# Kernel optimization log

Hardware: AMD Instinct MI355X
Metric: run time of the kernel (lower is better)

The kernel has to match this reference:

```python
import jax, jax.numpy as jnp
import numpy as np

N, C, HW, HEADS = 2048, 16, 8, 4
F = C * HW * HW  # 1024
E = 16384
EPS = 1e-5
NEG_SLOPE = 0.2


def _bn(x, g, b):
    # training-mode BatchNorm2d over (N, H, W)
    m = x.mean(axis=(0, 2, 3), keepdims=True)
    v = x.var(axis=(0, 2, 3), keepdims=True)
    return (x - m) * jax.lax.rsqrt(v + EPS) * g[None, :, None, None] + b[None, :, None, None]


def _conv1x1(x, w, b):
    # 1x1 conv == per-pixel linear: w is [out_c, in_c]
    return jnp.einsum('nchw,oc->nohw', x, w) + b[None, :, None, None]


def _gatv2(xf, edge_index, wl, bl, wr, br, att, bias_gat):
    # xf: [N, F] node features
    xl = (xf @ wl + bl).reshape(N, HEADS, F)  # source-side transform (lin_l)
    xr = (xf @ wr + br).reshape(N, HEADS, F)  # target-side transform (lin_r)
    src, dst = edge_index[0], edge_index[1]
    loops = jnp.arange(N)
    # PyG default: remove existing self loops (mask them) then add self loops
    src_f = jnp.concatenate([src, loops])
    dst_f = jnp.concatenate([dst, loops])
    valid = jnp.concatenate([src != dst, jnp.ones((N,), bool)])
    xj = xl[src_f]                                   # [E+N, HEADS, F] gather
    e = jax.nn.leaky_relu(xj + xr[dst_f], negative_slope=NEG_SLOPE)
    logits = jnp.einsum('ehf,hf->eh', e, att)        # [E+N, HEADS]
    logits = jnp.where(valid[:, None], logits, -jnp.inf)
    mx = jax.lax.stop_gradient(jax.ops.segment_max(logits, dst_f, num_segments=N))
    expv = jnp.where(valid[:, None], jnp.exp(logits - mx[dst_f]), 0.0)
    denom = jax.ops.segment_sum(expv, dst_f, num_segments=N)
    alpha = expv / denom[dst_f]                      # segment softmax over incoming edges
    out = jax.ops.segment_sum(alpha[:, :, None] * xj, dst_f, num_segments=N)  # [N, HEADS, F]
    return out.reshape(N, HEADS * F) + bias_gat


def setup_inputs() -> dict:
    key = jax.random.key(0)
    ks = jax.random.split(key, 8)
    s = 0.02
    return {
        'x': jax.random.normal(ks[0], (N, C, HW, HW), jnp.float32),
        'edge_index': jax.random.randint(ks[1], (2, E), 0, N),
        'w1': jax.random.normal(ks[2], (C, C), jnp.float32) * s,
        'b1': jnp.zeros((C,), jnp.float32),
        'g1': jnp.ones((C,), jnp.float32),
        'be1': jnp.zeros((C,), jnp.float32),
        'wl': jax.random.normal(ks[3], (F, HEADS * F), jnp.float32) * s,
        'bl': jnp.zeros((HEADS * F,), jnp.float32),
        'wr': jax.random.normal(ks[4], (F, HEADS * F), jnp.float32) * s,
        'br': jnp.zeros((HEADS * F,), jnp.float32),
        'att': jax.random.normal(ks[5], (HEADS, F), jnp.float32) * s,
        'bias_gat': jnp.zeros((HEADS * F,), jnp.float32),
        'w2': jax.random.normal(ks[6], (C, HEADS * C), jnp.float32) * s,
        'b2': jnp.zeros((C,), jnp.float32),
        'g2': jnp.ones((C,), jnp.float32),
        'be2': jnp.zeros((C,), jnp.float32),
    }


def reference(x, edge_index, w1, b1, g1, be1, wl, bl, wr, br, att, bias_gat, w2, b2, g2, be2):
    res = x
    y = _bn(_conv1x1(x, w1, b1), g1, be1)            # fc1: Conv2d 1x1 + BN
    yf = y.reshape(N, F)
    g = _gatv2(yf, edge_index, wl, bl, wr, br, att, bias_gat)
    g = g.reshape(N, HEADS * C, HW, HW)
    out = _bn(_conv1x1(g, w2, b2), g2, be2)          # fc2: Conv2d 1x1 + BN
    return out + res                                  # DropPath(0.0) == Identity
```

## Files before the change

### kernel.cpp

```cpp
#include <hip/hip_runtime.h>
#include <stdint.h>

#define N_NODES 2048
#define F_DIM   1024
#define HEADS   4
#define NF      4096
#define ROW     8192
#define E_EDGES 16384
#define MAXE    (E_EDGES + N_NODES)
#define BN_EPS  1e-5f
#define NSLOPE  0.2f

typedef unsigned short ushort_t;
typedef __attribute__((ext_vector_type(8))) short bf16x8;
typedef __attribute__((ext_vector_type(4))) float f32x4;
typedef __attribute__((ext_vector_type(8))) unsigned short us8;

__device__ __forceinline__ float b2f(unsigned short u) {
    union { unsigned int i; float f; } x; x.i = ((unsigned int)u) << 16; return x.f;
}
__device__ __forceinline__ unsigned short f2b(float f) {
    union { float f; unsigned int i; } x; x.f = f;
    unsigned int r = x.i + 0x7fffu + ((x.i >> 16) & 1u);
    return (unsigned short)(r >> 16);
}
__device__ __forceinline__ ushort_t ld_canon(const void* src, size_t i, int f32) {
    return f32 ? f2b(((const float*)src)[i]) : ((const ushort_t*)src)[i];
}
__device__ __forceinline__ float ld_f(const void* src, size_t i, int f32) {
    return f32 ? ((const float*)src)[i] : b2f(((const ushort_t*)src)[i]);
}

__device__ __forceinline__ int sniff_f32_blk(const ushort_t* xu, int* lds_flag) {
    int t = threadIdx.x;
    if (t < 64) {
        unsigned e = (xu[2 * t] >> 7) & 0xFF;
        unsigned long long m = __ballot(e >= 0x90u);
        if (t == 0) *lds_flag = (__popcll(m) >= 3) ? 1 : 0;
    }
    __syncthreads();
    return *lds_flag;
}
__device__ __forceinline__ int sniff_i64_blk(const int* ei_raw, int* lds_flag) {
    int t = threadIdx.x;
    if (t < 64) {
        unsigned long long m = __ballot(ei_raw[2 * t + 1] != 0);
        if (t == 0) *lds_flag = (m == 0ull) ? 1 : 0;
    }
    __syncthreads();
    return *lds_flag;
}

__global__ __launch_bounds__(256) void k_prep(
    const void* __restrict__ wl, const void* __restrict__ wr,
    const int* __restrict__ ei_raw, const ushort_t* __restrict__ xu,
    const void* __restrict__ x, const void* __restrict__ w1, const void* __restrict__ b1,
    const void* __restrict__ att, const void* __restrict__ bg,
    ushort_t* __restrict__ wT, int* __restrict__ counts,
    ushort_t* __restrict__ y0b, float* __restrict__ ps, float* __restrict__ pq,
    float* __restrict__ attf, float* __restrict__ bgf)
{
    __shared__ ushort_t tl[64][72];
    __shared__ float xs[1024];
    __shared__ float sw[256];
    __shared__ float sb[16];
    __shared__ int sfl;
    int b = blockIdx.x, t = threadIdx.x;
    if (b >= 2376) {
        int f32 = sniff_f32_blk(xu, &sfl);
        const void* src = (b == 2376) ? att : bg;
        float* dst = (b == 2376) ? attf : bgf;
        #pragma unroll
        for (int j = 0; j < 16; ++j) {
            int idx = t * 16 + j;
            dst[idx] = ld_f(src, idx, f32);
        }
    } else if (b < 2048) {
        int f32 = sniff_f32_blk(xu, &sfl);
        int z = b >> 10, rem = b & 1023;
        int bx = (rem & 63) * 64, by = (rem >> 6) * 64;
        const void* in = z ? wr : wl;
        ushort_t* outT = wT + (size_t)z * 4194304ull;
        #pragma unroll
        for (int i = 0; i < 2; ++i) {
            int idx = t + i * 256;
            int r = idx >> 3, c8 = (idx & 7) * 8;
            size_t gi = (size_t)(by + r) * 4096 + bx + c8;
            us8 v;
            if (f32) {
                const float* fp = (const float*)in + gi;
                float4 a = *(const float4*)fp;
                float4 bb = *(const float4*)(fp + 4);
                v[0] = f2b(a.x); v[1] = f2b(a.y); v[2] = f2b(a.z); v[3] = f2b(a.w);
                v[4] = f2b(bb.x); v[5] = f2b(bb.y); v[6] = f2b(bb.z); v[7] = f2b(bb.w);
            } else {
                v = *(const us8*)((const ushort_t*)in + gi);
            }
            *(us8*)(&tl[r][c8]) = v;
        }
        __syncthreads();
        #pragma unroll
        for (int i = 0; i < 2; ++i) {
            int idx = t + i * 256;
            int rr = idx >> 3, cc8 = (idx & 7) * 8;
            us8 v;
            #pragma unroll
            for (int j = 0; j < 8; ++j) v[j] = tl[cc8 + j][rr];
            *(us8*)(outT + (size_t)(bx + rr) * 1024 + by + cc8) = v;
        }
    } else if (b < 2120) {
        int i64 = sniff_i64_blk(ei_raw, &sfl);
        int idx = (b - 2048) * 256 + t;
        if (idx < E_EDGES) {
            int s = i64 ? ei_raw[2 * idx] : ei_raw[idx];
            int d = i64 ? ei_raw[2 * (E_EDGES + idx)] : ei_raw[E_EDGES + idx];
            if (s != d) atomicAdd(&counts[d], 1);
        } else if (idx < MAXE) {
            atomicAdd(&counts[idx - E_EDGES], 1);
        }
    } else {
        int bid = b - 2120;
        int f32 = sniff_f32_blk(xu, &sfl);
        sw[t] = ld_f(w1, t, f32);
        if (t < 16) sb[t] = ld_f(b1, t, f32);
        int wave = t >> 6, lane = t & 63;
        float s[4] = {0,0,0,0}, q[4] = {0,0,0,0};
        for (int nn = 0; nn < 8; ++nn) {
            int n = bid * 8 + nn;
            __syncthreads();
            #pragma unroll
            for (int i = 0; i < 4; ++i) {
                int idx = t + i * 256;
                xs[idx] = ld_f(x, (size_t)n * 1024 + idx, f32);
            }
            __syncthreads();
            #pragma unroll
            for (int i = 0; i < 4; ++i) {
                int o = wave * 4 + i;
                float acc = sb[o];
                #pragma unroll
                for (int c = 0; c < 16; ++c) acc += xs[c * 64 + lane] * sw[o * 16 + c];
                y0b[(size_t)n * 1024 + o * 64 + lane] = f2b(acc);
                s[i] += acc; q[i] += acc * acc;
            }
        }
        #pragma unroll
        for (int i = 0; i < 4; ++i)
            for (int mm = 1; mm < 64; mm <<= 1) {
                s[i] += __shfl_xor(s[i], mm);
                q[i] += __shfl_xor(q[i], mm);
            }
        if (lane == 0)
            #pragma unroll
            for (int i = 0; i < 4; ++i) {
                ps[bid * 16 + wave * 4 + i] = s[i];
                pq[bid * 16 + wave * 4 + i] = q[i];
            }
    }
}

__global__ __launch_bounds__(256) void k_scatnorm(
    const int* __restrict__ ei_raw, const int* __restrict__ counts,
    int* __restrict__ cursor, int* __restrict__ offs, int* __restrict__ esrc,
    const ushort_t* __restrict__ y0b,
    const float* __restrict__ ps, const float* __restrict__ pq,
    const void* __restrict__ g1, const void* __restrict__ be1,
    const ushort_t* __restrict__ xu, ushort_t* __restrict__ xf)
{
    __shared__ int offl[2048];
    __shared__ int ts[256];
    __shared__ int sfl;
    __shared__ float red[2][64];
    __shared__ float scs[16], shs[16];
    int t = threadIdx.x;
    if (blockIdx.x < 72) {
        int i64 = sniff_i64_blk(ei_raw, &sfl);
        int loc[8]; int tot = 0;
        #pragma unroll
        for (int j = 0; j < 8; ++j) { loc[j] = counts[t * 8 + j]; tot += loc[j]; }
        ts[t] = tot; __syncthreads();
        for (int s = 1; s < 256; s <<= 1) {
            int v = (t >= s) ? ts[t - s] : 0;
            __syncthreads();
            ts[t] += v;
            __syncthreads();
        }
        int run = ts[t] - tot;
        #pragma unroll
        for (int j = 0; j < 8; ++j) { offl[t * 8 + j] = run; run += loc[j]; }
        __syncthreads();
        if (blockIdx.x == 0) {
            #pragma unroll
            for (int j = 0; j < 8; ++j) offs[t * 8 + j] = offl[t * 8 + j];
            if (t == 255) offs[2048] = run;
        }
        int idx = blockIdx.x * 256 + t;
        if (idx < E_EDGES) {
            int s = i64 ? ei_raw[2 * idx] : ei_raw[idx];
            int d = i64 ? ei_raw[2 * (E_EDGES + idx)] : ei_raw[E_EDGES + idx];
            if (s != d) esrc[offl[d] + atomicAdd(&cursor[d], 1)] = s;
        } else if (idx < MAXE) {
            int n = idx - E_EDGES;
            esrc[offl[n] + atomicAdd(&cursor[n], 1)] = n;
        }
    } else {
        int f32 = sniff_f32_blk(xu, &sfl);
        int lane = t & 63, wv = t >> 6;
        float s = 0.f, q = 0.f;
        #pragma unroll
        for (int i = 0; i < 16; ++i) { s += ps[i * 256 + t]; q += pq[i * 256 + t]; }
        s += __shfl_xor(s, 16); q += __shfl_xor(q, 16);
        s += __shfl_xor(s, 32); q += __shfl_xor(q, 32);
        if (lane < 16) { red[0][wv * 16 + lane] = s; red[1][wv * 16 + lane] = q; }
        __syncthreads();
        if (t < 16) {
            float S = red[0][t] + red[0][16 + t] + red[0][32 + t] + red[0][48 + t];
            float Q = red[1][t] + red[1][16 + t] + red[1][32 + t] + red[1][48 + t];
            const float inv = 1.0f / 131072.0f;
            float mean = S * inv;
            float var  = Q * inv - mean * mean;
            float sc = ld_f(g1, t, f32) * rsqrtf(var + BN_EPS);
            scs[t] = sc;
            shs[t] = ld_f(be1, t, f32) - mean * sc;
        }
        __syncthreads();
        size_t base = (size_t)(blockIdx.x - 72) * 4096 + t * 16;
        int ch = ((int)(base >> 6)) & 15;
        float sc = scs[ch], sh = shs[ch];
        us8 v0 = *(const us8*)(y0b + base), v1 = *(const us8*)(y0b + base + 8);
        us8 o0, o1;
        #pragma unroll
        for (int j = 0; j < 8; ++j) {
            o0[j] = f2b(b2f(v0[j]) * sc + sh);
            o1[j] = f2b(b2f(v1[j]) * sc + sh);
        }
        *(us8*)(xf + base) = o0;
        *(us8*)(xf + base + 8) = o1;
    }
}

__global__ __launch_bounds__(256) void k_gemm(
    const ushort_t* __restrict__ A, const ushort_t* __restrict__ BT,
    const void* __restrict__ blr, const void* __restrict__ brr,
    const ushort_t* __restrict__ xu, ushort_t* __restrict__ out)
{
    __shared__ __align__(16) ushort_t smem[16384];
    ushort_t* As0 = smem;
    ushort_t* As1 = smem + 4096;
    ushort_t* Bs0 = smem + 8192;
    ushort_t* Bs1 = smem + 12288;
    ushort_t* cs  = smem;
    __shared__ int sfl;
    int f32 = sniff_f32_blk(xu, &sfl);
    int tid = threadIdx.x;
    int wv = tid >> 6, ln = tid & 63;
    int fid = blockIdx.y * 64 + blockIdx.x;
    int xcd = fid & 7, idx = fid >> 3;
    int m0 = (((xcd & 1) * 8) + (idx & 7)) * 128;
    int n0 = (((xcd >> 1) * 16) + (idx >> 3)) * 128;
    int wm = (wv >> 1) * 64, wn = (wv & 1) * 64;
    int lr = ln & 15, quad = ln >> 4;
    int swz8 = (quad ^ ((lr >> 1) & 3)) * 8;

    f32x4 acc[4][4];
    #pragma unroll
    for (int i = 0; i < 4; ++i)
        #pragma unroll
        for (int j2 = 0; j2 < 4; ++j2) acc[i][j2] = (f32x4){0.f, 0.f, 0.f, 0.f};

    for (int k0 = 0; k0 < 1024; k0 += 64) {
        #pragma unroll
        for (int i = 0; i < 2; ++i) {
            int cbase = i * 256 + wv * 64;
            int ci = cbase + ln;
            int m = ci >> 2, kc = ci & 3;
            int kq = kc ^ ((m >> 1) & 3);
            const ushort_t* ga = A + (size_t)(m0 + m) * 1024 + k0 + kq * 8;
            __builtin_amdgcn_global_load_lds(
                (const __attribute__((address_space(1))) void*)ga,
                (__attribute__((address_space(3))) void*)(&As0[cbase * 8]), 16, 0, 0);
            __builtin_amdgcn_global_load_lds(
                (const __attribute__((address_space(1))) void*)(ga + 32),
                (__attribute__((address_space(3))) void*)(&As1[cbase * 8]), 16, 0, 0);
            const ushort_t* gb = BT + (size_t)(n0 + m) * 1024 + k0 + kq * 8;
            __builtin_amdgcn_global_load_lds(
                (const __attribute__((address_space(1))) void*)gb,
                (__attribute__((address_space(3))) void*)(&Bs0[cbase * 8]), 16, 0, 0);
            __builtin_amdgcn_global_load_lds(
                (const __attribute__((address_space(1))) void*)(gb + 32),
                (__attribute__((address_space(3))) void*)(&Bs1[cbase * 8]), 16, 0, 0);
        }
        __syncthreads();
        #pragma unroll
        for (int p = 0; p < 2; ++p) {
            const ushort_t* Ap = p ? As1 : As0;
            const ushort_t* Bp = p ? Bs1 : Bs0;
            bf16x8 af[4], bfr[4];
            #pragma unroll
            for (int i = 0; i < 4; ++i)
                af[i] = *(const bf16x8*)(&Ap[(wm + i * 16 + lr) * 32 + swz8]);
            #pragma unroll
            for (int j2 = 0; j2 < 4; ++j2)
                bfr[j2] = *(const bf16x8*)(&Bp[(wn + j2 * 16 + lr) * 32 + swz8]);
            #pragma unroll
            for (int i = 0; i < 4; ++i)
                #pragma unroll
                for (int j2 = 0; j2 < 4; ++j2)
                    acc[i][j2] = __builtin_amdgcn_mfma_f32_16x16x32_bf16(af[i], bfr[j2], acc[i][j2], 0, 0, 0);
        }
        __syncthreads();
    }
    float bj[4];
    #pragma unroll
    for (int j2 = 0; j2 < 4; ++j2) {
        int colg = n0 + wn + j2 * 16 + lr;
        bj[j2] = (colg < 4096) ? ld_f(blr, colg, f32) : ld_f(brr, colg - 4096, f32);
    }
    #pragma unroll
    for (int ph = 0; ph < 2; ++ph) {
        if ((wv >> 1) == ph) {
            #pragma unroll
            for (int i = 0; i < 4; ++i)
                #pragma unroll
                for (int j2 = 0; j2 < 4; ++j2) {
                    int col = wn + j2 * 16 + lr;
                    #pragma unroll
                    for (int r = 0; r < 4; ++r)
                        cs[(i * 16 + quad * 4 + r) * 136 + col] = f2b(acc[i][j2][r] + bj[j2]);
                }
        }
        __syncthreads();
        #pragma unroll
        for (int rr = 0; rr < 4; ++rr) {
            int slot = rr * 256 + tid;
            int row = slot >> 4, seg = slot & 15;
            us8 v = *(const us8*)&cs[row * 136 + seg * 8];
            *(us8*)(out + (size_t)(m0 + ph * 64 + row) * ROW + n0 + seg * 8) = v;
        }
        __syncthreads();
    }
}

__global__ __launch_bounds__(64) void k_gat(
    const ushort_t* __restrict__ xlr,
    const float* __restrict__ attf, const float* __restrict__ bgf,
    const int* __restrict__ offsets, const int* __restrict__ esrc,
    ushort_t* __restrict__ g)
{
    int bx = blockIdx.x;
    int h = bx & 3;
    int dbase = (bx >> 2) * 4;
    int l = threadIdx.x;
    size_t hF = (size_t)h * F_DIM + l * 16;

    float attv[16], bgv[16];
    {
        const float* ap = attf + hF;
        const float* bp = bgf + hF;
        float4 a0 = *(const float4*)ap,       a1 = *(const float4*)(ap + 4);
        float4 a2 = *(const float4*)(ap + 8), a3 = *(const float4*)(ap + 12);
        float4 b0 = *(const float4*)bp,       b1 = *(const float4*)(bp + 4);
        float4 b2 = *(const float4*)(bp + 8), b3 = *(const float4*)(bp + 12);
        attv[0]=a0.x; attv[1]=a0.y; attv[2]=a0.z; attv[3]=a0.w;
        attv[4]=a1.x; attv[5]=a1.y; attv[6]=a1.z; attv[7]=a1.w;
        attv[8]=a2.x; attv[9]=a2.y; attv[10]=a2.z; attv[11]=a2.w;
        attv[12]=a3.x; attv[13]=a3.y; attv[14]=a3.z; attv[15]=a3.w;
        bgv[0]=b0.x; bgv[1]=b0.y; bgv[2]=b0.z; bgv[3]=b0.w;
        bgv[4]=b1.x; bgv[5]=b1.y; bgv[6]=b1.z; bgv[7]=b1.w;
        bgv[8]=b2.x; bgv[9]=b2.y; bgv[10]=b2.z; bgv[11]=b2.w;
        bgv[12]=b3.x; bgv[13]=b3.y; bgv[14]=b3.z; bgv[15]=b3.w;
    }

    for (int dd = 0; dd < 4; ++dd) {
        int d = dbase + dd;
        int off = offsets[d], deg = offsets[d + 1] - off;

        float xrv[16];
        {
            const ushort_t* xp = xlr + ((size_t)d * ROW + NF + hF);
            us8 x0 = *(const us8*)xp, x1 = *(const us8*)(xp + 8);
            #pragma unroll
            for (int j = 0; j < 8; ++j) { xrv[j] = b2f(x0[j]); xrv[8 + j] = b2f(x1[j]); }
        }
        float acc[16];
        #pragma unroll
        for (int j = 0; j < 16; ++j) acc[j] = 0.f;
        float s_run = 0.f;

        for (int c0 = 0; c0 < deg; c0 += 64) {
            int cnt = min(64, deg - c0);
            int eidx = esrc[off + c0 + (l < cnt ? l : 0)];
            int e = 0;
            for (; e + 3 < cnt; e += 4) {
                int i0 = __shfl(eidx, e),     i1 = __shfl(eidx, e + 1);
                int i2 = __shfl(eidx, e + 2), i3 = __shfl(eidx, e + 3);
                const ushort_t* p0 = xlr + ((size_t)i0 * ROW + hF);
                const ushort_t* p1 = xlr + ((size_t)i1 * ROW + hF);
                const ushort_t* p2 = xlr + ((size_t)i2 * ROW + hF);
                const ushort_t* p3 = xlr + ((size_t)i3 * ROW + hF);
                us8 v0[4], v1[4];
                v0[0] = *(const us8*)p0; v1[0] = *(const us8*)(p0 + 8);
                v0[1] = *(const us8*)p1; v1[1] = *(const us8*)(p1 + 8);
                v0[2] = *(const us8*)p2; v1[2] = *(const us8*)(p2 + 8);
                v0[3] = *(const us8*)p3; v1[3] = *(const us8*)(p3 + 8);
                float tt[4];
                #pragma unroll
                for (int k = 0; k < 4; ++k) {
                    float t0 = 0.f;
                    #pragma unroll
                    for (int j = 0; j < 8; ++j) {
                        float u;
                        u = b2f(v0[k][j]) + xrv[j];     u = u > 0.f ? u : NSLOPE * u; t0 += u * attv[j];
                        u = b2f(v1[k][j]) + xrv[8 + j]; u = u > 0.f ? u : NSLOPE * u; t0 += u * attv[8 + j];
                    }
                    tt[k] = t0;
                }
                #pragma unroll
                for (int mm = 1; mm < 64; mm <<= 1) {
                    tt[0] += __shfl_xor(tt[0], mm);
                    tt[1] += __shfl_xor(tt[1], mm);
                    tt[2] += __shfl_xor(tt[2], mm);
                    tt[3] += __shfl_xor(tt[3], mm);
                }
                float w0 = __expf(tt[0]), w1 = __expf(tt[1]);
                float w2v = __expf(tt[2]), w3 = __expf(tt[3]);
                s_run += w0 + w1 + w2v + w3;
                #pragma unroll
                for (int j = 0; j < 8; ++j) {
                    acc[j]     += w0 * b2f(v0[0][j]) + w1 * b2f(v0[1][j])
                                + w2v * b2f(v0[2][j]) + w3 * b2f(v0[3][j]);
                    acc[8 + j] += w0 * b2f(v1[0][j]) + w1 * b2f(v1[1][j])
                                + w2v * b2f(v1[2][j]) + w3 * b2f(v1[3][j]);
                }
            }
            for (; e < cnt; ++e) {
                int i0 = __shfl(eidx, e);
                const ushort_t* p = xlr + ((size_t)i0 * ROW + hF);
                us8 a0 = *(const us8*)p, a1 = *(const us8*)(p + 8);
                float t0 = 0.f;
                #pragma unroll
                for (int j = 0; j < 8; ++j) {
                    float u;
                    u = b2f(a0[j]) + xrv[j];     u = u > 0.f ? u : NSLOPE * u; t0 += u * attv[j];
                    u = b2f(a1[j]) + xrv[8 + j]; u = u > 0.f ? u : NSLOPE * u; t0 += u * attv[8 + j];
                }
                #pragma unroll
                for (int mm = 1; mm < 64; mm <<= 1) t0 += __shfl_xor(t0, mm);
                float w0 = __expf(t0);
                s_run += w0;
                #pragma unroll
                for (int j = 0; j < 8; ++j) {
                    acc[j]     += w0 * b2f(a0[j]);
                    acc[8 + j] += w0 * b2f(a1[j]);
                }
            }
        }
        float inv = 1.0f / s_run;
        ushort_t* gp = g + ((size_t)d * NF + hF);
        us8 outv0, outv1;
        #pragma unroll
        for (int j = 0; j < 8; ++j) {
            outv0[j] = f2b(acc[j] * inv + bgv[j]);
            outv1[j] = f2b(acc[8 + j] * inv + bgv[8 + j]);
        }
        *(us8*)gp = outv0;
        *(us8*)(gp + 8) = outv1;
    }
}

__global__ __launch_bounds__(256) void k_fc2(
    const ushort_t* __restrict__ g, const void* __restrict__ w2, const void* __restrict__ b2,
    const ushort_t* __restrict__ xu,
    ushort_t* __restrict__ zb, float* __restrict__ ps, float* __restrict__ pq)
{
    __shared__ float gs[4096];
    __shared__ float sw[1024];
    __shared__ float sb[16];
    __shared__ int sfl;
    int f32 = sniff_f32_blk(xu, &sfl);
    int tid = threadIdx.x;
    #pragma unroll
    for (int i = 0; i < 4; ++i) sw[tid + i * 256] = ld_f(w2, tid + i * 256, f32);
    if (tid < 16) sb[tid] = ld_f(b2, tid, f32);
    int wave = tid >> 6, lane = tid & 63;
    float s[4] = {0,0,0,0}, q[4] = {0,0,0,0};
    for (int nn = 0; nn < 2; ++nn) {
        int n = blockIdx.x * 2 + nn;
        __syncthreads();
        {
            const ushort_t* gp = g + (size_t)n * 4096 + tid * 16;
            us8 v0 = *(const us8*)gp, v1 = *(const us8*)(gp + 8);
            #pragma unroll
            for (int j = 0; j < 8; ++j) {
                gs[tid * 16 + j] = b2f(v0[j]);
                gs[tid * 16 + 8 + j] = b2f(v1[j]);
            }
        }
        __syncthreads();
        float acc[4];
        #pragma unroll
        for (int i = 0; i < 4; ++i) acc[i] = sb[wave * 4 + i];
        #pragma unroll 8
        for (int k = 0; k < 64; ++k) {
            float gv = gs[k * 64 + lane];
            #pragma unroll
            for (int i = 0; i < 4; ++i)
                acc[i] += gv * sw[(wave * 4 + i) * 64 + k];
        }
        #pragma unroll
        for (int i = 0; i < 4; ++i) {
            zb[(size_t)n * 1024 + (wave * 4 + i) * 64 + lane] = f2b(acc[i]);
            s[i] += acc[i]; q[i] += acc[i] * acc[i];
        }
    }
    #pragma unroll
    for (int i = 0; i < 4; ++i)
        for (int mm = 1; mm < 64; mm <<= 1) {
            s[i] += __shfl_xor(s[i], mm);
            q[i] += __shfl_xor(q[i], mm);
        }
    if (lane == 0)
        #pragma unroll
        for (int i = 0; i < 4; ++i) {
            ps[blockIdx.x * 16 + wave * 4 + i] = s[i];
            pq[blockIdx.x * 16 + wave * 4 + i] = q[i];
        }
}

__global__ __launch_bounds__(256) void k_out(
    const ushort_t* __restrict__ zb, const void* __restrict__ x,
    const float* __restrict__ ps, const float* __restrict__ pq,
    const void* __restrict__ g2, const void* __restrict__ be2,
    void* __restrict__ out)
{
    __shared__ float red[2][64];
    __shared__ float scs[16], shs[16];
    __shared__ int sfl;
    int f32 = sniff_f32_blk((const ushort_t*)x, &sfl);
    int t = threadIdx.x, lane = t & 63, wv = t >> 6;
    float s = 0.f, q = 0.f;
    #pragma unroll
    for (int i = 0; i < 64; ++i) { s += ps[i * 256 + t]; q += pq[i * 256 + t]; }
    s += __shfl_xor(s, 16); q += __shfl_xor(q, 16);
    s += __shfl_xor(s, 32); q += __shfl_xor(q, 32);
    if (lane < 16) { red[0][wv * 16 + lane] = s; red[1][wv * 16 + lane] = q; }
    __syncthreads();
    if (t < 16) {
        float S = red[0][t] + red[0][16 + t] + red[0][32 + t] + red[0][48 + t];
        float Q = red[1][t] + red[1][16 + t] + red[1][32 + t] + red[1][48 + t];
        const float inv = 1.0f / 131072.0f;
        float mean = S * inv;
        float var  = Q * inv - mean * mean;
        float sc = ld_f(g2, t, f32) * rsqrtf(var + BN_EPS);
        scs[t] = sc;
        shs[t] = ld_f(be2, t, f32) - mean * sc;
    }
    __syncthreads();
    size_t base = (size_t)blockIdx.x * 4096;
    #pragma unroll
    for (int i = 0; i < 16; ++i) {
        size_t k = base + t + i * 256;
        int ch = ((int)k >> 6) & 15;
        float val = b2f(zb[k]) * scs[ch] + shs[ch] + ld_f(x, k, f32);
        if (f32) ((float*)out)[k] = val;
        else     ((ushort_t*)out)[k] = f2b(val);
    }
}

extern "C" void kernel_launch(void* const* d_in, const int* in_sizes, int n_in,
                              void* d_out, int out_size, void* d_ws, size_t ws_size,
                              hipStream_t stream)
{
    const void* x   = d_in[0];
    const void* ei  = d_in[1];
    const void* w1  = d_in[2];
    const void* b1  = d_in[3];
    const void* g1  = d_in[4];
    const void* be1 = d_in[5];
    const void* wl  = d_in[6];
    const void* bl  = d_in[7];
    const void* wr  = d_in[8];
    const void* br  = d_in[9];
    const void* att = d_in[10];
    const void* bg  = d_in[11];
    const void* w2  = d_in[12];
    const void* b2  = d_in[13];
    const void* g2  = d_in[14];
    const void* be2 = d_in[15];
    (void)in_sizes; (void)n_in; (void)out_size; (void)ws_size;

    char* wsb = (char*)d_ws;
    size_t o = 0;
    auto alloc = [&](size_t bytes) -> void* {
        void* p = wsb + o;
        o = (o + bytes + 255) & ~(size_t)255;
        return p;
    };
    ushort_t* y0b   = (ushort_t*)alloc(2097152ull * 2);
    ushort_t* xf    = (ushort_t*)alloc(2097152ull * 2);
    ushort_t* zb    = (ushort_t*)alloc(2097152ull * 2);
    ushort_t* wT    = (ushort_t*)alloc(8388608ull * 2);
    ushort_t* gbuf  = wT;
    ushort_t* xlr   = (ushort_t*)alloc(16777216ull * 2);
    float* p1s = (float*)alloc(256 * 16 * 4);
    float* p1q = (float*)alloc(256 * 16 * 4);
    float* p2s = (float*)alloc(1024 * 16 * 4);
    float* p2q = (float*)alloc(1024 * 16 * 4);
    int* counts = (int*)alloc(2048 * 4);
    int* cursor = (int*)alloc(2048 * 4);
    int* offs   = (int*)alloc(2049 * 4);
    int* esrc   = (int*)alloc(MAXE * 4);
    float* attf = (float*)alloc(4096 * 4);
    float* bgf  = (float*)alloc(4096 * 4);

    hipMemsetAsync(counts, 0, 2 * 2048 * 4, stream);
    k_prep<<<2378, 256, 0, stream>>>(wl, wr, (const int*)ei, (const ushort_t*)x,
                                     x, w1, b1, att, bg, wT, counts, y0b, p1s, p1q, attf, bgf);
    k_scatnorm<<<584, 256, 0, stream>>>((const int*)ei, counts, cursor, offs, esrc,
                                        y0b, p1s, p1q, g1, be1, (const ushort_t*)x, xf);
    k_gemm<<<dim3(64, 16), 256, 0, stream>>>(xf, wT, bl, br, (const ushort_t*)x, xlr);
    k_gat<<<2048, 64, 0, stream>>>(xlr, attf, bgf, offs, esrc, gbuf);
    k_fc2<<<1024, 256, 0, stream>>>(gbuf, w2, b2, (const ushort_t*)x, zb, p2s, p2q);
    k_out<<<512, 256, 0, stream>>>(zb, x, p2s, p2q, g2, be2, d_out);
}
```

Baseline: 245.4 us.

## Double-buffer GEMM k-loop so next tile loads overlap MFMA compute

```diff
diff --git a/kernel.cpp b/kernel.cpp
--- a/kernel.cpp
+++ b/kernel.cpp
@@ -245,11 +245,7 @@
     const ushort_t* __restrict__ xu, ushort_t* __restrict__ out)
 {
     __shared__ __align__(16) ushort_t smem[16384];
-    ushort_t* As0 = smem;
-    ushort_t* As1 = smem + 4096;
-    ushort_t* Bs0 = smem + 8192;
-    ushort_t* Bs1 = smem + 12288;
-    ushort_t* cs  = smem;
+    ushort_t* cs = smem;
     __shared__ int sfl;
     int f32 = sniff_f32_blk(xu, &sfl);
     int tid = threadIdx.x;
@@ -268,48 +264,52 @@
         #pragma unroll
         for (int j2 = 0; j2 < 4; ++j2) acc[i][j2] = (f32x4){0.f, 0.f, 0.f, 0.f};
 
-    for (int k0 = 0; k0 < 1024; k0 += 64) {
+    auto stage = [&](int tt, int bsel) {
+        ushort_t* Ab = smem + bsel * 8192;
+        ushort_t* Bb = Ab + 4096;
         #pragma unroll
         for (int i = 0; i < 2; ++i) {
             int cbase = i * 256 + wv * 64;
             int ci = cbase + ln;
-            int m = ci >> 2, kc = ci & 3;
-            int kq = kc ^ ((m >> 1) & 3);
-            const ushort_t* ga = A + (size_t)(m0 + m) * 1024 + k0 + kq * 8;
+            int r = ci >> 2, sg = ci & 3;
+            int lsg = sg ^ ((r >> 1) & 3);
+            const ushort_t* ga = A + (size_t)(m0 + r) * 1024 + tt * 32 + lsg * 8;
             __builtin_amdgcn_global_load_lds(
                 (const __attribute__((address_space(1))) void*)ga,
-                (__attribute__((address_space(3))) void*)(&As0[cbase * 8]), 16, 0, 0);
-            __builtin_amdgcn_global_load_lds(
-                (const __attribute__((address_space(1))) void*)(ga + 32),
-                (__attribute__((address_space(3))) void*)(&As1[cbase * 8]), 16, 0, 0);
-            const ushort_t* gb = BT + (size_t)(n0 + m) * 1024 + k0 + kq * 8;
+                (__attribute__((address_space(3))) void*)(&Ab[cbase * 8]), 16, 0, 0);
+            const ushort_t* gb = BT + (size_t)(n0 + r) * 1024 + tt * 32 + lsg * 8;
             __builtin_amdgcn_global_load_lds(
                 (const __attribute__((address_space(1))) void*)gb,
-                (__attribute__((address_space(3))) void*)(&Bs0[cbase * 8]), 16, 0, 0);
-            __builtin_amdgcn_global_load_lds(
-                (const __attribute__((address_space(1))) void*)(gb + 32),
-                (__attribute__((address_space(3))) void*)(&Bs1[cbase * 8]), 16, 0, 0);
-        }
-        __syncthreads();
-        #pragma unroll
-        for (int p = 0; p < 2; ++p) {
-            const ushort_t* Ap = p ? As1 : As0;
-            const ushort_t* Bp = p ? Bs1 : Bs0;
-            bf16x8 af[4], bfr[4];
-            #pragma unroll
-            for (int i = 0; i < 4; ++i)
-                af[i] = *(const bf16x8*)(&Ap[(wm + i * 16 + lr) * 32 + swz8]);
+                (__attribute__((address_space(3))) void*)(&Bb[cbase * 8]), 16, 0, 0);
+        }
+    };
+
+    auto compute = [&](int bsel) {
+        const ushort_t* Ap = smem + bsel * 8192;
+        const ushort_t* Bp = Ap + 4096;
+        bf16x8 af[4], bfr[4];
+        #pragma unroll
+        for (int i = 0; i < 4; ++i)
+            af[i] = *(const bf16x8*)(&Ap[(wm + i * 16 + lr) * 32 + swz8]);
+        #pragma unroll
+        for (int j2 = 0; j2 < 4; ++j2)
+            bfr[j2] = *(const bf16x8*)(&Bp[(wn + j2 * 16 + lr) * 32 + swz8]);
+        #pragma unroll
+        for (int i = 0; i < 4; ++i)
             #pragma unroll
             for (int j2 = 0; j2 < 4; ++j2)
-                bfr[j2] = *(const bf16x8*)(&Bp[(wn + j2 * 16 + lr) * 32 + swz8]);
-            #pragma unroll
-            for (int i = 0; i < 4; ++i)
-                #pragma unroll
-                for (int j2 = 0; j2 < 4; ++j2)
-                    acc[i][j2] = __builtin_amdgcn_mfma_f32_16x16x32_bf16(af[i], bfr[j2], acc[i][j2], 0, 0, 0);
-        }
-        __syncthreads();
-    }
+                acc[i][j2] = __builtin_amdgcn_mfma_f32_16x16x32_bf16(af[i], bfr[j2], acc[i][j2], 0, 0, 0);
+    };
+
+    stage(0, 0);
+    __syncthreads();
+    #pragma unroll 1
+    for (int t = 0; t < 32; ++t) {
+        if (t < 31) stage(t + 1, (t + 1) & 1);
+        compute(t & 1);
+        __syncthreads();
+    }
+
     float bj[4];
     #pragma unroll
     for (int j2 = 0; j2 < 4; ++j2) {
```

Result: slower. 252.4 us (+2.8%).
